# Kernel tuning notes

Measured on AMD Instinct MI355X. Metric: run time of the kernel, lower is better.

The kernel has to match this reference:

```python
import jax, jax.numpy as jnp
import numpy as np

LORA_R = 32
LORA_ALPHA = 64
SCALING = LORA_ALPHA / LORA_R  # LoraLinear.scaling_
INIT_STD = 0.02  # router_init_range_


def setup_inputs() -> dict:
    key = jax.random.key(0)
    k0, k1, k2, k3, k4 = jax.random.split(key, 5)
    B, S, D, O, E, R = 4, 4096, 3072, 3072, 8, LORA_R
    x = jax.random.normal(k0, (B, S, D), jnp.float32)
    W = jax.random.normal(k1, (O, D), jnp.float32) * INIT_STD          # base_layer weight
    gate_w = jax.random.normal(k2, (E, D), jnp.float32) * INIT_STD     # router gate
    lora_A = jax.random.normal(k3, (E, R, D), jnp.float32) * INIT_STD  # per-expert lora_A.weight
    lora_B = jax.random.normal(k4, (E, O, R), jnp.float32) * INIT_STD  # per-expert lora_B.weight
    return {"x": x, "W": W, "gate_w": gate_w, "lora_A": lora_A, "lora_B": lora_B, "top_k": 2}


def reference(x, W, gate_w, lora_A, lora_B, top_k):
    # MixLoRA routing: softmax gate -> top-k -> renormalize -> per-expert LoRA -> combine.
    B, S, D = x.shape
    E = gate_w.shape[0]
    xt = x.reshape(-1, D)                       # [T, D], T = B*S
    residual = xt @ W.T                         # base_layer(hidden_states)
    logits = xt @ gate_w.T                      # [T, E]
    probs = jax.nn.softmax(logits, axis=-1)
    top_w, top_i = jax.lax.top_k(probs, top_k)  # [T, k]
    top_w = top_w / top_w.sum(-1, keepdims=True)
    # per-token per-expert combine weight (0 for unselected experts) [T, E]
    oh = jax.nn.one_hot(top_i, E, dtype=xt.dtype)          # [T, k, E]
    w_te = jnp.einsum('tke,tk->te', oh, top_w)             # [T, E]
    # dense-dispatch equivalent of gather/scatter: unselected experts have weight 0
    a = jnp.einsum('td,erd->ter', xt, lora_A)              # [T, E, R]  (dropout = identity, eval)
    y = jnp.einsum('ter,eor,te->to', a, lora_B, w_te)      # [T, O]
    out = residual + SCALING * y
    return out.reshape(B, S, -1)
```

## Files before the change

kernel.cpp:

```cpp
#include <hip/hip_runtime.h>
#include <hip/hip_bf16.h>
#include <stdint.h>

typedef unsigned short u16;
typedef __attribute__((ext_vector_type(8))) short short8;
typedef __attribute__((ext_vector_type(4))) float floatx4;

#define T_NUM 16384
#define D_DIM 3072
#define O_DIM 3072
#define E_NUM 8
#define R_DIM 32
#define KA    (E_NUM * R_DIM)

__device__ __forceinline__ float bf2f(u16 u) {
    union { unsigned int i; float f; } v;
    v.i = ((unsigned int)u) << 16;
    return v.f;
}
__device__ __forceinline__ u16 f2bf(float f) {
    union { float f; unsigned int u; } v;
    v.f = f;
    unsigned int r = (v.u + 0x7FFFu + ((v.u >> 16) & 1u)) >> 16;
    return (u16)r;
}

struct f8 { float v[8]; };

template<bool BF>
__device__ __forceinline__ f8 loadf8(const void* p, size_t idx) {
    f8 r;
    if constexpr (BF) {
        short8 s = *(const short8*)((const u16*)p + idx);
#pragma unroll
        for (int j = 0; j < 8; ++j) r.v[j] = bf2f((u16)s[j]);
    } else {
        const float* f = (const float*)p + idx;
        floatx4 a = *(const floatx4*)f;
        floatx4 b = *(const floatx4*)(f + 4);
#pragma unroll
        for (int j = 0; j < 4; ++j) { r.v[j] = a[j]; r.v[4 + j] = b[j]; }
    }
    return r;
}

template<bool BF>
__device__ __forceinline__ short8 load8bf(const void* p, size_t idx) {
    if constexpr (BF) {
        return *(const short8*)((const u16*)p + idx);
    } else {
        const float* f = (const float*)p + idx;
        floatx4 a = *(const floatx4*)f;
        floatx4 b = *(const floatx4*)(f + 4);
        short8 s;
#pragma unroll
        for (int j = 0; j < 4; ++j) { s[j] = (short)f2bf(a[j]); s[4 + j] = (short)f2bf(b[j]); }
        return s;
    }
}

__global__ void detect_kernel(const u16* __restrict__ x16, int* __restrict__ flag) {
    __shared__ int cnt;
    if (threadIdx.x == 0) cnt = 0;
    __syncthreads();
    int local = 0;
#pragma unroll
    for (int i = 0; i < 32; ++i) {
        u16 u = x16[(size_t)(threadIdx.x * 32 + i) * 2];
        int e = (u >> 7) & 0xFF;
        local += (e < 100 || e > 150) ? 1 : 0;
    }
    atomicAdd(&cnt, local);
    __syncthreads();
    if (threadIdx.x == 0) *flag = (cnt < 2048) ? 1 : 0;
}

__global__ __launch_bounds__(256) void cvt_kernel(
    const float* __restrict__ src, u16* __restrict__ dst, int n8,
    const int* __restrict__ flag, int want)
{
    if (*flag != want) return;
    int idx = blockIdx.x * 256 + threadIdx.x;
    if (idx >= n8) return;
    short8 s = load8bf<false>(src, (size_t)idx * 8);
    *(short8*)(dst + (size_t)idx * 8) = s;
}

template<bool BF>
__global__ __launch_bounds__(256) void routing_kernel(
    const void* __restrict__ x, const void* __restrict__ gate_w,
    float* __restrict__ s_te, u16* __restrict__ xb,
    const int* __restrict__ flag, int want)
{
    if (*flag != want) return;
    int lane = threadIdx.x & 63;
    int wave = threadIdx.x >> 6;
    int t = blockIdx.x * 4 + wave;

    float acc[E_NUM];
#pragma unroll
    for (int e = 0; e < E_NUM; ++e) acc[e] = 0.f;

#pragma unroll
    for (int i = 0; i < 6; ++i) {
        size_t d = (size_t)(i * 64 + lane) * 8;
        f8 xv = loadf8<BF>(x, (size_t)t * D_DIM + d);
        if constexpr (!BF) {
            if (xb) {
                short8 s;
#pragma unroll
                for (int j = 0; j < 8; ++j) s[j] = (short)f2bf(xv.v[j]);
                *(short8*)(xb + (size_t)t * D_DIM + d) = s;
            }
        }
#pragma unroll
        for (int e = 0; e < E_NUM; ++e) {
            f8 gv = loadf8<BF>(gate_w, (size_t)e * D_DIM + d);
#pragma unroll
            for (int j = 0; j < 8; ++j) acc[e] += xv.v[j] * gv.v[j];
        }
    }
#pragma unroll
    for (int e = 0; e < E_NUM; ++e) {
#pragma unroll
        for (int off = 32; off > 0; off >>= 1)
            acc[e] += __shfl_xor(acc[e], off, 64);
    }
    if (lane == 0) {
        int i0 = 0; float l0 = acc[0];
        for (int e = 1; e < E_NUM; ++e) if (acc[e] > l0) { l0 = acc[e]; i0 = e; }
        int i1 = -1; float l1 = -1e30f;
        for (int e = 0; e < E_NUM; ++e) if (e != i0 && acc[e] > l1) { l1 = acc[e]; i1 = e; }
        float w0 = 1.f / (1.f + __expf(l1 - l0));
        float w1 = 1.f - w0;
        float s[E_NUM];
#pragma unroll
        for (int e = 0; e < E_NUM; ++e) s[e] = 0.f;
        s[i0] = 2.f * w0;
        s[i1] = 2.f * w1;
#pragma unroll
        for (int e = 0; e < E_NUM; ++e) s_te[(size_t)t * E_NUM + e] = s[e];
    }
}

template<bool BF>
__global__ __launch_bounds__(256) void pack_b_kernel(
    const void* __restrict__ loraB, u16* __restrict__ Bp,
    const int* __restrict__ flag, int want)
{
    if (*flag != want) return;
    int idx = blockIdx.x * 256 + threadIdx.x;
    int e = idx / O_DIM;
    int o = idx - e * O_DIM;
#pragma unroll
    for (int i = 0; i < 4; ++i) {
        short8 s = load8bf<BF>(loraB, (size_t)idx * R_DIM + i * 8);
        *(short8*)(Bp + (size_t)o * KA + e * R_DIM + i * 8) = s;
    }
}

template<bool BF1, bool OUTBF>
__global__ __launch_bounds__(256) void gemm_kernel(
    const void* __restrict__ A1, int lda1, int kt1,
    const u16* __restrict__ A2, int lda2, int kt2,
    const void* __restrict__ B1, int ldb1,
    const u16* __restrict__ B2, int ldb2,
    void* __restrict__ outv, int ldo,
    const float* __restrict__ s_te, int scale_mode,
    const int* __restrict__ flag, int want)
{
    if (*flag != want) return;
    __shared__ short As[2][128 * 64];
    __shared__ short Bs[2][128 * 64];

    const int tid  = threadIdx.x;
    const int lane = tid & 63;
    const int wave = tid >> 6;
    const int rowA0 = blockIdx.x * 128;
    const int rowB0 = blockIdx.y * 128;

    floatx4 acc[4][4];
#pragma unroll
    for (int mi = 0; mi < 4; ++mi)
#pragma unroll
        for (int ni = 0; ni < 4; ++ni)
            acc[mi][ni] = (floatx4){0.f, 0.f, 0.f, 0.f};

    const int m_base = (wave & 1) * 64;
    const int n_base = (wave >> 1) * 64;
    const int quad = lane >> 4;
    const int r16  = lane & 15;

    int srow[4], scol[4], soff[4];
#pragma unroll
    for (int i = 0; i < 4; ++i) {
        int c = wave * 256 + i * 64 + lane;
        int r = c >> 3, c8 = c & 7;
        srow[i] = r;
        scol[i] = c8 * 8;
        soff[i] = r * 64 + ((c8 ^ (r & 7)) * 8);
    }

    auto LD = [&](int kt, short8 av[4], short8 bv[4]) {
        if (kt < kt1) {
            const int ko = kt * 64;
#pragma unroll
            for (int i = 0; i < 4; ++i) {
                av[i] = load8bf<BF1>(A1, (size_t)(rowA0 + srow[i]) * lda1 + ko + scol[i]);
                bv[i] = load8bf<BF1>(B1, (size_t)(rowB0 + srow[i]) * ldb1 + ko + scol[i]);
            }
        } else {
            const int ko = (kt - kt1) * 64;
#pragma unroll
            for (int i = 0; i < 4; ++i) {
                av[i] = *(const short8*)(A2 + (size_t)(rowA0 + srow[i]) * lda2 + ko + scol[i]);
                bv[i] = *(const short8*)(B2 + (size_t)(rowB0 + srow[i]) * ldb2 + ko + scol[i]);
            }
        }
    };
    auto ST = [&](int buf, const short8 av[4], const short8 bv[4]) {
#pragma unroll
        for (int i = 0; i < 4; ++i) {
            *(short8*)(&As[buf][soff[i]]) = av[i];
            *(short8*)(&Bs[buf][soff[i]]) = bv[i];
        }
    };

    const int ktot = kt1 + kt2;
    short8 pa[4], pb[4];
    LD(0, pa, pb);
    ST(0, pa, pb);
    __syncthreads();
    int cur = 0;

    for (int kt = 0; kt < ktot; ++kt) {
        const bool more = (kt + 1 < ktot);
        if (more) LD(kt + 1, pa, pb);

#pragma unroll
        for (int kk = 0; kk < 64; kk += 32) {
            short8 af[4], bfg[4];
#pragma unroll
            for (int mi = 0; mi < 4; ++mi) {
                const int row = m_base + mi * 16 + r16;
                af[mi] = *(const short8*)(&As[cur][row * 64 + ((kk + quad * 8) ^ ((row & 7) * 8))]);
            }
#pragma unroll
            for (int ni = 0; ni < 4; ++ni) {
                const int row = n_base + ni * 16 + r16;
                bfg[ni] = *(const short8*)(&Bs[cur][row * 64 + ((kk + quad * 8) ^ ((row & 7) * 8))]);
            }
#pragma unroll
            for (int mi = 0; mi < 4; ++mi)
#pragma unroll
                for (int ni = 0; ni < 4; ++ni)
                    acc[mi][ni] = __builtin_amdgcn_mfma_f32_16x16x32_bf16(
                        af[mi], bfg[ni], acc[mi][ni], 0, 0, 0);
        }

        if (more) {
            ST(cur ^ 1, pa, pb);
            __syncthreads();
            cur ^= 1;
        }
    }

#pragma unroll
    for (int mi = 0; mi < 4; ++mi) {
#pragma unroll
        for (int r = 0; r < 4; ++r) {
            int t = rowA0 + m_base + mi * 16 + quad * 4 + r;
#pragma unroll
            for (int ni = 0; ni < 4; ++ni) {
                int o = rowB0 + n_base + ni * 16 + r16;
                float v = acc[mi][ni][r];
                if (scale_mode) v *= s_te[(size_t)t * E_NUM + (o >> 5)];
                if constexpr (OUTBF)
                    ((u16*)outv)[(size_t)t * ldo + o] = f2bf(v);
                else
                    ((float*)outv)[(size_t)t * ldo + o] = v;
            }
        }
    }
}

extern "C" void kernel_launch(void* const* d_in, const int* in_sizes, int n_in,
                              void* d_out, int out_size, void* d_ws, size_t ws_size,
                              hipStream_t stream)
{
    const void* x      = d_in[0];
    const void* W      = d_in[1];
    const void* gate_w = d_in[2];
    const void* lora_A = d_in[3];
    const void* lora_B = d_in[4];

    int*   flag     = (int*)d_ws;
    float* s_te     = (float*)((char*)d_ws + 1024);
    u16*   a_scaled = (u16*)((char*)d_ws + 1024 + 524288);
    u16*   B_pack   = (u16*)((char*)d_ws + 1024 + 524288 + 8388608);
    const size_t base_sz = 1024 + 524288 + 8388608 + 1572864;

    const size_t x16_sz = (size_t)T_NUM * D_DIM * 2;
    const size_t W16_sz = (size_t)O_DIM * D_DIM * 2;
    const size_t A16_sz = (size_t)KA * D_DIM * 2;
    const bool big = ws_size >= base_sz + x16_sz + W16_sz + A16_sz;
    u16* x16 = big ? (u16*)((char*)d_ws + base_sz) : nullptr;
    u16* W16 = big ? (u16*)((char*)x16 + x16_sz)   : nullptr;
    u16* A16 = big ? (u16*)((char*)W16 + W16_sz)   : nullptr;

    detect_kernel<<<1, 256, 0, stream>>>((const u16*)x, flag);

    routing_kernel<true ><<<T_NUM / 4, 256, 0, stream>>>(x, gate_w, s_te, nullptr, flag, 1);
    routing_kernel<false><<<T_NUM / 4, 256, 0, stream>>>(x, gate_w, s_te, x16, flag, 0);

    pack_b_kernel<true ><<<(E_NUM * O_DIM) / 256, 256, 0, stream>>>(lora_B, B_pack, flag, 1);
    pack_b_kernel<false><<<(E_NUM * O_DIM) / 256, 256, 0, stream>>>(lora_B, B_pack, flag, 0);

    gemm_kernel<true, true><<<dim3(T_NUM / 128, KA / 128), 256, 0, stream>>>(
        x, D_DIM, D_DIM / 64, (const u16*)x, D_DIM, 0,
        lora_A, D_DIM, (const u16*)lora_A, D_DIM,
        a_scaled, KA, s_te, 1, flag, 1);
    gemm_kernel<true, true><<<dim3(T_NUM / 128, O_DIM / 128), 256, 0, stream>>>(
        x, D_DIM, D_DIM / 64, a_scaled, KA, KA / 64,
        W, D_DIM, B_pack, KA,
        d_out, O_DIM, nullptr, 0, flag, 1);

    if (big) {
        cvt_kernel<<<(O_DIM * D_DIM / 8 + 255) / 256, 256, 0, stream>>>(
            (const float*)W, W16, O_DIM * D_DIM / 8, flag, 0);
        cvt_kernel<<<(KA * D_DIM / 8 + 255) / 256, 256, 0, stream>>>(
            (const float*)lora_A, A16, KA * D_DIM / 8, flag, 0);

        gemm_kernel<true, true><<<dim3(T_NUM / 128, KA / 128), 256, 0, stream>>>(
            x16, D_DIM, D_DIM / 64, x16, D_DIM, 0,
            A16, D_DIM, A16, D_DIM,
            a_scaled, KA, s_te, 1, flag, 0);
        gemm_kernel<true, false><<<dim3(T_NUM / 128, O_DIM / 128), 256, 0, stream>>>(
            x16, D_DIM, D_DIM / 64, a_scaled, KA, KA / 64,
            W16, D_DIM, B_pack, KA,
            d_out, O_DIM, nullptr, 0, flag, 0);
    } else {
        gemm_kernel<false, true><<<dim3(T_NUM / 128, KA / 128), 256, 0, stream>>>(
            x, D_DIM, D_DIM / 64, (const u16*)x, D_DIM, 0,
            lora_A, D_DIM, (const u16*)lora_A, D_DIM,
            a_scaled, KA, s_te, 1, flag, 0);
        gemm_kernel<false, false><<<dim3(T_NUM / 128, O_DIM / 128), 256, 0, stream>>>(
            x, D_DIM, D_DIM / 64, a_scaled, KA, KA / 64,
            W, D_DIM, B_pack, KA,
            d_out, O_DIM, nullptr, 0, flag, 0);
    }
}
```

Before: 862.6 us.

## Add 256x256-tile GEMM with direct global-to-LDS loads for main fused GEMM

Adds a new GEMM kernel with 256x256 output tiles, 512 threads and 128KB of dynamic LDS. It uses global_load_lds for asynchronous loads, XOR-swizzled LDS, double buffering and a phased pipeline that interleaves the next tile's loads with MFMA work under barriers and setprio. A block swizzle is applied for L2 locality. The kernel replaces the 128x128 GEMM for the base+LoRA output product in the bf16 and big-workspace paths, aiming for more data reuse per tile and better load/compute overlap. The larger tiles raise register and LDS pressure and allow fewer blocks per CU.

Measured after the change: 831.0 us. -3.7%, faster.

```diff
diff --git a/kernel.cpp b/kernel.cpp
--- a/kernel.cpp
+++ b/kernel.cpp
@@ -58,6 +58,15 @@
         return s;
     }
 }
+
+__device__ __forceinline__ void gload16(const u16* g, const short* l) {
+    __builtin_amdgcn_global_load_lds(
+        (const __attribute__((address_space(1))) void*)g,
+        (__attribute__((address_space(3))) void*)l, 16, 0, 0);
+}
+
+#define BARR  asm volatile("s_barrier" ::: "memory")
+#define LGKM0 asm volatile("s_waitcnt lgkmcnt(0)" ::: "memory")
 
 __global__ void detect_kernel(const u16* __restrict__ x16, int* __restrict__ flag) {
     __shared__ int cnt;
@@ -284,6 +293,160 @@
     }
 }
 
+template<bool OUTBF>
+__global__ __launch_bounds__(512, 2) void gemm256_kernel(
+    const u16* __restrict__ A1, int lda1, int kt1,
+    const u16* __restrict__ A2, int lda2, int kt2,
+    const u16* __restrict__ B1, int ldb1,
+    const u16* __restrict__ B2, int ldb2,
+    void* __restrict__ outv, int ldo,
+    const int* __restrict__ flag, int want)
+{
+    if (*flag != want) return;
+    extern __shared__ short smem[];
+
+    const int tid  = threadIdx.x;
+    const int lane = tid & 63;
+    const int wave = tid >> 6;
+    const int wm   = wave >> 2;
+    const int wn   = wave & 3;
+    const int quad = lane >> 4;
+    const int r16  = lane & 15;
+    const int rb   = lane >> 3;
+    const int swz  = (lane & 7) ^ rb;
+
+    const int lin = blockIdx.y * 64 + blockIdx.x;
+    const int sw  = (lin & 7) * 96 + (lin >> 3);
+    const int rowA0 = (sw & 63) * 256;
+    const int rowB0 = (sw >> 6) * 256;
+
+    floatx4 acc[8][4];
+#pragma unroll
+    for (int mi = 0; mi < 8; ++mi)
+#pragma unroll
+        for (int ni = 0; ni < 4; ++ni)
+            acc[mi][ni] = (floatx4){0.f, 0.f, 0.f, 0.f};
+
+    const int ktot = kt1 + kt2;
+
+    auto stA = [&](int nb, int q, int ks) {
+        const u16* g;
+        if (ks < kt1) g = A1 + (size_t)(rowA0 + q * 8 + rb) * lda1 + (size_t)ks * 64 + swz * 8;
+        else          g = A2 + (size_t)(rowA0 + q * 8 + rb) * lda2 + (size_t)(ks - kt1) * 64 + swz * 8;
+        gload16(g, smem + nb * 16384 + q * 512);
+    };
+    auto stB = [&](int nb, int q, int ks) {
+        const u16* g;
+        if (ks < kt1) g = B1 + (size_t)(rowB0 + q * 8 + rb) * ldb1 + (size_t)ks * 64 + swz * 8;
+        else          g = B2 + (size_t)(rowB0 + q * 8 + rb) * ldb2 + (size_t)(ks - kt1) * 64 + swz * 8;
+        gload16(g, smem + 32768 + nb * 16384 + q * 512);
+    };
+
+    stB(0, wave, 0); stB(0, 8 + wave, 0); stB(0, 16 + wave, 0); stB(0, 24 + wave, 0);
+    stA(0, wave, 0); stA(0, 8 + wave, 0); stA(0, 16 + wave, 0); stA(0, 24 + wave, 0);
+    asm volatile("s_waitcnt vmcnt(0)" ::: "memory");
+    BARR;
+
+    int cur = 0;
+    short8 bf[4][2];
+
+    for (int kt = 0; kt < ktot; ++kt) {
+        const int  ks   = kt + 1;
+        const bool more = ks < ktot;
+        const int  nb   = cur ^ 1;
+        const short* Acur = smem + cur * 16384;
+        const short* Bcur = smem + 32768 + cur * 16384;
+
+        auto rdA = [&](int p, short8 af[2][2]) {
+#pragma unroll
+            for (int m2 = 0; m2 < 2; ++m2) {
+                const int rowm = wm * 128 + (2 * p + m2) * 16 + r16;
+                const int sx = rowm & 7;
+#pragma unroll
+                for (int kx = 0; kx < 2; ++kx)
+                    af[m2][kx] = *(const short8*)(Acur + rowm * 64 + (((quad + 4 * kx) ^ sx) * 8));
+            }
+        };
+        auto domfma = [&](int p, short8 af[2][2]) {
+#pragma unroll
+            for (int m2 = 0; m2 < 2; ++m2)
+#pragma unroll
+                for (int kx = 0; kx < 2; ++kx)
+#pragma unroll
+                    for (int ni = 0; ni < 4; ++ni)
+                        acc[2 * p + m2][ni] = __builtin_amdgcn_mfma_f32_16x16x32_bf16(
+                            af[m2][kx], bf[ni][kx], acc[2 * p + m2][ni], 0, 0, 0);
+        };
+
+        short8 af[2][2];
+
+        rdA(0, af);
+#pragma unroll
+        for (int ni = 0; ni < 4; ++ni) {
+            const int rown = wn * 64 + ni * 16 + r16;
+            const int sx = rown & 7;
+#pragma unroll
+            for (int kx = 0; kx < 2; ++kx)
+                bf[ni][kx] = *(const short8*)(Bcur + rown * 64 + (((quad + 4 * kx) ^ sx) * 8));
+        }
+        if (more) { stB(nb, wave, ks); stB(nb, 8 + wave, ks); }
+        BARR; LGKM0;
+        __builtin_amdgcn_s_setprio(1);
+        domfma(0, af);
+        __builtin_amdgcn_s_setprio(0);
+        BARR;
+
+        rdA(1, af);
+        if (more) {
+            stB(nb, 16 + wave, ks); stB(nb, 24 + wave, ks);
+            stA(nb, wave, ks);      stA(nb, 16 + wave, ks);
+            asm volatile("s_waitcnt vmcnt(6)" ::: "memory");
+        } else {
+            asm volatile("s_waitcnt vmcnt(0)" ::: "memory");
+        }
+        BARR; LGKM0;
+        __builtin_amdgcn_s_setprio(1);
+        domfma(1, af);
+        __builtin_amdgcn_s_setprio(0);
+        BARR;
+
+        rdA(2, af);
+        if (more) { stA(nb, 8 + wave, ks); stA(nb, 24 + wave, ks); }
+        BARR; LGKM0;
+        __builtin_amdgcn_s_setprio(1);
+        domfma(2, af);
+        __builtin_amdgcn_s_setprio(0);
+        BARR;
+
+        rdA(3, af);
+        if (more) asm volatile("s_waitcnt vmcnt(2)" ::: "memory");
+        BARR; LGKM0;
+        __builtin_amdgcn_s_setprio(1);
+        domfma(3, af);
+        __builtin_amdgcn_s_setprio(0);
+        BARR;
+
+        cur = nb;
+    }
+
+#pragma unroll
+    for (int mi = 0; mi < 8; ++mi) {
+#pragma unroll
+        for (int r = 0; r < 4; ++r) {
+            const int t = rowA0 + wm * 128 + mi * 16 + quad * 4 + r;
+#pragma unroll
+            for (int ni = 0; ni < 4; ++ni) {
+                const int o = rowB0 + wn * 64 + ni * 16 + r16;
+                float v = acc[mi][ni][r];
+                if constexpr (OUTBF)
+                    ((u16*)outv)[(size_t)t * ldo + o] = f2bf(v);
+                else
+                    ((float*)outv)[(size_t)t * ldo + o] = v;
+            }
+        }
+    }
+}
+
 extern "C" void kernel_launch(void* const* d_in, const int* in_sizes, int n_in,
                               void* d_out, int out_size, void* d_ws, size_t ws_size,
                               hipStream_t stream)
@@ -308,6 +471,11 @@
     u16* W16 = big ? (u16*)((char*)x16 + x16_sz)   : nullptr;
     u16* A16 = big ? (u16*)((char*)W16 + W16_sz)   : nullptr;
 
+    (void)hipFuncSetAttribute((const void*)gemm256_kernel<true>,
+                              hipFuncAttributeMaxDynamicSharedMemorySize, 131072);
+    (void)hipFuncSetAttribute((const void*)gemm256_kernel<false>,
+                              hipFuncAttributeMaxDynamicSharedMemorySize, 131072);
+
     detect_kernel<<<1, 256, 0, stream>>>((const u16*)x, flag);
 
     routing_kernel<true ><<<T_NUM / 4, 256, 0, stream>>>(x, gate_w, s_te, nullptr, flag, 1);
@@ -315,15 +483,17 @@
 
     pack_b_kernel<true ><<<(E_NUM * O_DIM) / 256, 256, 0, stream>>>(lora_B, B_pack, flag, 1);
     pack_b_kernel<false><<<(E_NUM * O_DIM) / 256, 256, 0, stream>>>(lora_B, B_pack, flag, 0);
+
+    const dim3 g2(T_NUM / 256, O_DIM / 256);
 
     gemm_kernel<true, true><<<dim3(T_NUM / 128, KA / 128), 256, 0, stream>>>(
         x, D_DIM, D_DIM / 64, (const u16*)x, D_DIM, 0,
         lora_A, D_DIM, (const u16*)lora_A, D_DIM,
         a_scaled, KA, s_te, 1, flag, 1);
-    gemm_kernel<true, true><<<dim3(T_NUM / 128, O_DIM / 128), 256, 0, stream>>>(
-        x, D_DIM, D_DIM / 64, a_scaled, KA, KA / 64,
-        W, D_DIM, B_pack, KA,
-        d_out, O_DIM, nullptr, 0, flag, 1);
+    gemm256_kernel<true><<<g2, 512, 131072, stream>>>(
+        (const u16*)x, D_DIM, D_DIM / 64, a_scaled, KA, KA / 64,
+        (const u16*)W, D_DIM, B_pack, KA,
+        d_out, O_DIM, flag, 1);
 
     if (big) {
         cvt_kernel<<<(O_DIM * D_DIM / 8 + 255) / 256, 256, 0, stream>>>(
@@ -335,17 +505,17 @@
             x16, D_DIM, D_DIM / 64, x16, D_DIM, 0,
             A16, D_DIM, A16, D_DIM,
             a_scaled, KA, s_te, 1, flag, 0);
-        gemm_kernel<true, false><<<dim3(T_NUM / 128, O_DIM / 128), 256, 0, stream>>>(
+        gemm256_kernel<false><<<g2, 512, 131072, stream>>>(
             x16, D_DIM, D_DIM / 64, a_scaled, KA, KA / 64,
             W16, D_DIM, B_pack, KA,
-            d_out, O_DIM, nullptr, 0, flag, 0);
+            d_out, O_DIM, flag, 0);
     } else {
         gemm_kernel<false, true><<<dim3(T_NUM / 128, KA / 128), 256, 0, stream>>>(
             x, D_DIM, D_DIM / 64, (const u16*)x, D_DIM, 0,
             lora_A, D_DIM, (const u16*)lora_A, D_DIM,
             a_scaled, KA, s_te, 1, flag, 0);
         gemm_kernel<false, false><<<dim3(T_NUM / 128, O_DIM / 128), 256, 0, stream>>>(
-            x, D_DIM, D_DIM / 64, a_scaled, KA, KA / 64,
+            x, D_DIM, D_DIM / 64, a_scaled, KA, 4,
             W, D_DIM, B_pack, KA,
             d_out, O_DIM, nullptr, 0, flag, 0);
     }
```
